# Kernel optimization log

Hardware: AMD Instinct MI355X
Metric: run time of the kernel (lower is better)

## Reference

```python
import jax, jax.numpy as jnp
import numpy as np

H = 16      # num_attention_heads
HD = 32     # attention_head_size
W = 7       # window size (per side)
N = W * W   # tokens per window = 49
MW = 64     # windows per image (mask_shape)
C = H * HD  # dim = 512
B = 2048    # total windows = images * MW


def _relative_position_index():
    coords = np.stack(np.meshgrid(np.arange(W), np.arange(W), indexing='ij'))  # [2,W,W]
    cf = coords.reshape(2, -1)                      # [2, N]
    rel = cf[:, :, None] - cf[:, None, :]           # [2, N, N]
    rel = rel.transpose(1, 2, 0).copy()             # [N, N, 2]
    rel[:, :, 0] += W - 1
    rel[:, :, 1] += W - 1
    rel[:, :, 0] *= 2 * W - 1
    return jnp.asarray(rel.sum(-1), dtype=jnp.int32)  # [N, N] indices into bias table

REL_IDX = _relative_position_index()


def setup_inputs() -> dict:
    key = jax.random.key(0)
    ks = jax.random.split(key, 9)
    s = 0.02
    return {
        "hidden_states": jax.random.normal(ks[0], (B, N, C), jnp.float32),
        "attention_mask": jax.random.normal(ks[1], (MW, N, N), jnp.float32),
        "wq": jax.random.normal(ks[2], (C, C), jnp.float32) * s,
        "bq": jax.random.normal(ks[3], (C,), jnp.float32) * s,
        "wk": jax.random.normal(ks[4], (C, C), jnp.float32) * s,
        "bk": jax.random.normal(ks[5], (C,), jnp.float32) * s,
        "wv": jax.random.normal(ks[6], (C, C), jnp.float32) * s,
        "bv": jax.random.normal(ks[7], (C,), jnp.float32) * s,
        "bias_table": jax.random.normal(ks[8], ((2 * W - 1) ** 2, H), jnp.float32) * s,
    }


def reference(hidden_states, attention_mask, wq, bq, wk, bk, wv, bv, bias_table):
    # hidden_states: [B, N, C]
    def proj(w, b):
        y = hidden_states @ w.T + b                  # [B, N, C]
        return y.reshape(B, N, H, HD).transpose(0, 2, 1, 3)  # [B, H, N, HD]

    q = proj(wq, bq)
    k = proj(wk, bk)
    v = proj(wv, bv)

    inv_sqrt_d = 1.0 / jnp.sqrt(jnp.float32(HD))
    scores = jnp.einsum('bhnd,bhmd->bhnm', q, k) * inv_sqrt_d  # [B, H, N, N]

    # relative position bias gather: [N, N, H] -> [H, N, N]
    rel_bias = bias_table[REL_IDX].transpose(2, 0, 1)
    scores = scores + rel_bias[None]

    # shifted-window mask: broadcast over image groups and heads
    scores = scores.reshape(B // MW, MW, H, N, N) + attention_mask[None, :, None]
    scores = scores.reshape(B, H, N, N)

    probs = jax.nn.softmax(scores, axis=-1)
    ctx = jnp.einsum('bhnm,bhmd->bhnd', probs, v)    # [B, H, N, HD]
    return ctx.transpose(0, 2, 1, 3).reshape(B, N, C)
```

## Files before the change

### kernel.cpp

```cpp
#include <hip/hip_runtime.h>
#include <hip/hip_bf16.h>
#include <string.h>

typedef unsigned short u16;
typedef __attribute__((ext_vector_type(8))) short short8;
typedef __attribute__((ext_vector_type(4))) float floatx4;
typedef __attribute__((ext_vector_type(4))) unsigned short ushort4v;
typedef __attribute__((ext_vector_type(8))) unsigned short ushort8v;
typedef __attribute__((ext_vector_type(2))) unsigned int uint2v;

#define NWIN 2048
#define NTOK 49
#define NH 16
#define HDIM 32
#define CDIM 512
#define MTOT (NWIN * NTOK)
#define NOUT (3 * CDIM)
#define KDIM CDIM

__device__ inline float b2f(u16 u) {
    unsigned int x = ((unsigned int)u) << 16;
    float f; __builtin_memcpy(&f, &x, 4); return f;
}
__device__ inline u16 f2b(float f) {
    unsigned int u; __builtin_memcpy(&u, &f, 4);
    unsigned int r = (u + 0x7fffu + ((u >> 16) & 1u)) >> 16;
    return (u16)r;
}
__device__ inline void gload16(const void* g, void* l) {
    __builtin_amdgcn_global_load_lds((const __attribute__((address_space(1))) unsigned int*)g,
                                     (__attribute__((address_space(3))) unsigned int*)l, 16, 0, 0);
}

__global__ void k_cvt_x(const float4* __restrict__ x, ushort4v* __restrict__ xb, int n4) {
    int i = blockIdx.x * blockDim.x + threadIdx.x;
    int stride = gridDim.x * blockDim.x;
    for (; i < n4; i += stride) {
        float4 v = x[i];
        ushort4v o = { f2b(v.x), f2b(v.y), f2b(v.z), f2b(v.w) };
        xb[i] = o;
    }
}

__global__ void k_pack_w(const float* __restrict__ wq, const float* __restrict__ wk,
                         const float* __restrict__ wv, const float* __restrict__ bq,
                         const float* __restrict__ bk, const float* __restrict__ bv,
                         u16* __restrict__ wout, float* __restrict__ bout) {
    const int WN = CDIM * CDIM;
    int i = blockIdx.x * blockDim.x + threadIdx.x;
    if (i < 3 * WN) {
        const float* src = (i < WN) ? wq : (i < 2 * WN ? wk : wv);
        wout[i] = f2b(src[i & (WN - 1)]);
    }
    if (i < 3 * CDIM) {
        const float* sb = (i < CDIM) ? bq : (i < 2 * CDIM ? bk : bv);
        bout[i] = sb[i & (CDIM - 1)];
    }
}

__global__ void k_bm(const float* __restrict__ mask, const float* __restrict__ bt,
                     float* __restrict__ bm) {
    int t = blockIdx.x;
    int w = t >> 4, h = t & 15;
    for (int e = threadIdx.x; e < NTOK * NTOK; e += blockDim.x) {
        int j = e / 49, i = e - j * 49;
        int ri = i / 7, ci = i - ri * 7;
        int rj = j / 7, cj = j - rj * 7;
        int idx = (ri - rj + 6) * 13 + (ci - cj + 6);
        bm[(size_t)t * 2401 + e] = bt[idx * 16 + h] + mask[(size_t)w * 2401 + i * 49 + j];
    }
}

__global__ __launch_bounds__(512, 2)
void k_gemm256(const u16* __restrict__ A, const u16* __restrict__ Bw,
               const float* __restrict__ bias, u16* __restrict__ C) {
    __shared__ __align__(16) u16 lds[65536];
    const int tid = threadIdx.x;
    const int lane = tid & 63;
    const int wave = tid >> 6;
    const int wm = wave >> 2;
    const int wn = wave & 3;
    const int c = lane & 15;
    const int quad = lane >> 4;

    const int wg = blockIdx.x;
    const int swz = (wg & 7) * 294 + (wg >> 3);
    const int m0 = (swz / 6) * 256;
    const int n0 = (swz % 6) * 256;

    const int r1 = tid >> 3;
    const int cg = ((tid & 7) ^ (r1 & 7)) * 8;
    const int bpr = (r1 & 15) * 4 + (r1 >> 4);
    const u16* pA00 = A + (size_t)(m0 + r1) * KDIM + cg;
    const u16* pA01 = A + (size_t)(m0 + 64 + r1) * KDIM + cg;
    const u16* pA10 = A + (size_t)(m0 + 128 + r1) * KDIM + cg;
    const u16* pA11 = A + (size_t)(m0 + 192 + r1) * KDIM + cg;
    const u16* pB00 = Bw + (size_t)(n0 + bpr) * KDIM + cg;
    const u16* pB01 = Bw + (size_t)(n0 + 64 + bpr) * KDIM + cg;
    const u16* pB10 = Bw + (size_t)(n0 + 128 + bpr) * KDIM + cg;
    const u16* pB11 = Bw + (size_t)(n0 + 192 + bpr) * KDIM + cg;

#define STG(P0, P1, BUFU, HALFU, KOFF) \
    gload16(P0 + (KOFF), lds + (BUFU) + (HALFU) + tid * 8); \
    gload16(P1 + (KOFF), lds + (BUFU) + (HALFU) + 4096 + tid * 8);
#define STG_A0(T)  STG(pA00, pA01, 0, 0, (T)*64)
#define STG_A1(T)  STG(pA10, pA11, 0, 8192, (T)*64)
#define STG_B0(T)  STG(pB00, pB01, 0, 16384, (T)*64)
#define STG_B1(T)  STG(pB10, pB11, 0, 24576, (T)*64)
#define STG_A0b(T) STG(pA00, pA01, 32768, 0, (T)*64)
#define STG_A1b(T) STG(pA10, pA11, 32768, 8192, (T)*64)
#define STG_B0b(T) STG(pB00, pB01, 32768, 16384, (T)*64)
#define STG_B1b(T) STG(pB10, pB11, 32768, 24576, (T)*64)

    const char* ldsc = (const char*)lds;
    const int aBase = wm * 16384;
    const int bBase = 32768 + (wn >> 1) * 16384 + (wn & 1) * 8192;
    const int cx = (c & 7) << 4;
    const int kq0 = (quad * 16) ^ cx;
    const int kq1 = (64 + quad * 16) ^ cx;

    short8 af[4][2];
    short8 bf[2][2][2];
    floatx4 acc[8][4];
#pragma unroll
    for (int mf = 0; mf < 8; mf++)
#pragma unroll
        for (int nf = 0; nf < 4; nf++)
            acc[mf][nf] = (floatx4){0.f, 0.f, 0.f, 0.f};

#define LDA(BUF, MH) { _Pragma("unroll") for (int mi = 0; mi < 4; mi++) { \
        const char* pp_ = ldsc + (BUF)*65536 + aBase + (MH)*8192 + (mi*16 + c)*128; \
        af[mi][0] = *(const short8*)(pp_ + kq0); \
        af[mi][1] = *(const short8*)(pp_ + kq1); } }
#define LDB(BUF, NH) { _Pragma("unroll") for (int ni = 0; ni < 2; ni++) { \
        const char* pp_ = ldsc + (BUF)*65536 + bBase + (NH)*4096 + (ni*16 + c)*128; \
        bf[NH][ni][0] = *(const short8*)(pp_ + kq0); \
        bf[NH][ni][1] = *(const short8*)(pp_ + kq1); } }
#define BAR __builtin_amdgcn_s_barrier()
#define WAITLGKM { asm volatile("s_waitcnt lgkmcnt(0)" ::: "memory"); __builtin_amdgcn_sched_barrier(0); }
#define MQ(MH, NH) do { __builtin_amdgcn_s_setprio(1); \
    _Pragma("unroll") for (int kk = 0; kk < 2; kk++) \
    _Pragma("unroll") for (int mi = 0; mi < 4; mi++) \
    _Pragma("unroll") for (int ni = 0; ni < 2; ni++) \
        acc[(MH)*4 + mi][(NH)*2 + ni] = __builtin_amdgcn_mfma_f32_16x16x32_bf16( \
            af[mi][kk], bf[NH][ni][kk], acc[(MH)*4 + mi][(NH)*2 + ni], 0, 0, 0); \
    __builtin_amdgcn_s_setprio(0); } while (0)

#define GITER(T2, T3, ST, VM4) \
     LDA(0,0); LDB(0,0);                               BAR; WAITLGKM; MQ(0,0); BAR; \
     LDB(0,1);                                         BAR; WAITLGKM; MQ(0,1); BAR; \
     LDA(0,1); if (ST) { STG_B0(T2); }                 BAR; WAITLGKM; MQ(1,0); BAR; \
     if (ST) { STG_B1(T2); STG_A0(T2); }               BAR; WAITLGKM; MQ(1,1); \
            asm volatile("s_waitcnt " VM4 ::: "memory");      BAR; \
     LDA(1,0); LDB(1,0); if (ST) { STG_A1(T2); }       BAR; WAITLGKM; MQ(0,0); BAR; \
     LDB(1,1);                                         BAR; WAITLGKM; MQ(0,1); BAR; \
     LDA(1,1); if (ST) { STG_B0b(T3); }                BAR; WAITLGKM; MQ(1,0); BAR; \
     if (ST) { STG_B1b(T3); STG_A0b(T3); STG_A1b(T3); } BAR; WAITLGKM; MQ(1,1); \
            if (ST) { asm volatile("s_waitcnt vmcnt(8)" ::: "memory"); } BAR;

    STG_A0(0); STG_A1(0); STG_B0(0); STG_B1(0);
    STG_A0b(1); STG_A1b(1); STG_B0b(1); STG_B1b(1);
    asm volatile("s_waitcnt vmcnt(8)" ::: "memory");
    BAR;

    GITER(2, 3, 1, "vmcnt(6)")
    GITER(4, 5, 1, "vmcnt(6)")
    GITER(6, 7, 1, "vmcnt(6)")
    GITER(8, 9, 0, "vmcnt(0)")

    const float4 bb = *(const float4*)&bias[n0 + wn * 64 + c * 4];
    u16* cbase = C + (size_t)(m0 + wm * 128 + quad * 4) * NOUT + n0 + wn * 64 + c * 4;
#pragma unroll
    for (int mf = 0; mf < 8; mf++) {
#pragma unroll
        for (int r = 0; r < 4; r++) {
            float x0 = acc[mf][0][r] + bb.x;
            float x1 = acc[mf][1][r] + bb.y;
            float x2 = acc[mf][2][r] + bb.z;
            float x3 = acc[mf][3][r] + bb.w;
            unsigned int d0, d1;
            asm("v_cvt_pk_bf16_f32 %0, %1, %2" : "=v"(d0) : "v"(x0), "v"(x1));
            asm("v_cvt_pk_bf16_f32 %0, %1, %2" : "=v"(d1) : "v"(x2), "v"(x3));
            uint2v w2 = { d0, d1 };
            *(uint2v*)(cbase + (size_t)(mf * 16 + r) * NOUT) = w2;
        }
    }
#undef STG
#undef STG_A0
#undef STG_A1
#undef STG_B0
#undef STG_B1
#undef STG_A0b
#undef STG_A1b
#undef STG_B0b
#undef STG_B1b
#undef LDA
#undef LDB
#undef BAR
#undef WAITLGKM
#undef MQ
#undef GITER
}

__global__ __launch_bounds__(256, 3)
void k_attn(const u16* __restrict__ qkv, const float* __restrict__ bmT,
            float* __restrict__ out) {
    __shared__ __align__(16) char smem[4 * 12288];
    const int lane = threadIdx.x & 63;
    const int wave = threadIdx.x >> 6;
    const int task = blockIdx.x * 4 + wave;
    const int b = task >> 4;
    const int h = task & 15;
    const int c = lane & 15;
    const int quad = lane >> 4;
    char* Vs = smem + wave * 12288;
    char* Ps = Vs + 4096;

    const u16* qbase = qkv + (size_t)b * NTOK * NOUT + h * 32;

    short8 kf[4], qf[4];
#pragma unroll
    for (int mi = 0; mi < 4; mi++) {
        int jr = mi * 16 + c; jr = jr > 48 ? 48 : jr;
        kf[mi] = *(const short8*)(qbase + (size_t)jr * NOUT + 512 + quad * 8);
    }
#pragma unroll
    for (int ni = 0; ni < 4; ni++) {
        int ir = ni * 16 + c; ir = ir > 48 ? 48 : ir;
        qf[ni] = *(const short8*)(qbase + (size_t)ir * NOUT + quad * 8);
    }

#pragma unroll
    for (int it = 0; it < 4; it++) {
        int j = it * 16 + (lane >> 2);
        int part = lane & 3;
        ushort8v val = {0, 0, 0, 0, 0, 0, 0, 0};
        if (j < 49) val = *(const ushort8v*)(qbase + (size_t)j * NOUT + 1024 + part * 8);
        int byt = (j * 64 + part * 16) ^ (((j >> 3) & 3) << 4);
        *(ushort8v*)(Vs + byt) = val;
    }

    floatx4 acc[4][4];
#pragma unroll
    for (int mi = 0; mi < 4; mi++)
#pragma unroll
        for (int ni = 0; ni < 4; ni++)
            acc[mi][ni] = (floatx4){0.f, 0.f, 0.f, 0.f};
#pragma unroll
    for (int mi = 0; mi < 4; mi++)
#pragma unroll
        for (int ni = 0; ni < 4; ni++)
            acc[mi][ni] = __builtin_amdgcn_mfma_f32_16x16x32_bf16(kf[mi], qf[ni], acc[mi][ni], 0, 0, 0);

    const float scale = 0.17677669529663687f;
    const float* bmrow = bmT + ((size_t)((b & 63) * 16 + h)) * 2401;
#pragma unroll
    for (int mi = 0; mi < 4; mi++)
#pragma unroll
        for (int r = 0; r < 4; r++) {
            int j = mi * 16 + quad * 4 + r;
            int jc = j > 48 ? 48 : j;
            const float* bp = bmrow + jc * 49;
#pragma unroll
            for (int ni = 0; ni < 4; ni++) {
                int i = ni * 16 + c;
                int ic = i > 48 ? 48 : i;
                acc[mi][ni][r] = acc[mi][ni][r] * scale + bp[ic];
            }
        }

#pragma unroll
    for (int ni = 0; ni < 4; ni++) {
        float mx = -3.0e38f;
#pragma unroll
        for (int mi = 0; mi < 3; mi++)
#pragma unroll
            for (int r = 0; r < 4; r++) mx = fmaxf(mx, acc[mi][ni][r]);
        if (quad == 0) mx = fmaxf(mx, acc[3][ni][0]);
        mx = fmaxf(mx, __shfl_xor(mx, 16));
        mx = fmaxf(mx, __shfl_xor(mx, 32));
        float sum = 0.f;
#pragma unroll
        for (int mi = 0; mi < 3; mi++)
#pragma unroll
            for (int r = 0; r < 4; r++) {
                float e = __expf(acc[mi][ni][r] - mx);
                acc[mi][ni][r] = e; sum += e;
            }
        float e0 = (quad == 0) ? __expf(acc[3][ni][0] - mx) : 0.f;
        acc[3][ni][0] = e0; sum += e0;
        acc[3][ni][1] = 0.f; acc[3][ni][2] = 0.f; acc[3][ni][3] = 0.f;
        sum += __shfl_xor(sum, 16);
        sum += __shfl_xor(sum, 32);
        float inv = 1.0f / sum;
#pragma unroll
        for (int mi = 0; mi < 4; mi++)
#pragma unroll
            for (int r = 0; r < 4; r++) acc[mi][ni][r] *= inv;
    }

    const int cx = (c & 7) << 4;
#pragma unroll
    for (int ni = 0; ni < 4; ni++) {
        char* prow = Ps + (ni * 16 + c) * 128;
#pragma unroll
        for (int mi = 0; mi < 4; mi++) {
            unsigned int d0, d1;
            asm("v_cvt_pk_bf16_f32 %0, %1, %2" : "=v"(d0) : "v"(acc[mi][ni][0]), "v"(acc[mi][ni][1]));
            asm("v_cvt_pk_bf16_f32 %0, %1, %2" : "=v"(d1) : "v"(acc[mi][ni][2]), "v"(acc[mi][ni][3]));
            uint2v w2 = { d0, d1 };
            *(uint2v*)(prow + ((mi * 32 + quad * 8) ^ cx)) = w2;
        }
    }

    asm volatile("s_waitcnt lgkmcnt(0)" ::: "memory");

    floatx4 acc2[4][2];
#pragma unroll
    for (int mi = 0; mi < 4; mi++)
#pragma unroll
        for (int ni = 0; ni < 2; ni++) acc2[mi][ni] = (floatx4){0.f, 0.f, 0.f, 0.f};
    const int vb0 = quad * 512 + (((0 * 16 + c) * 2) ^ (quad << 4));
    const int vb1 = quad * 512 + (((1 * 16 + c) * 2) ^ (quad << 4));
#pragma unroll
    for (int kk = 0; kk < 2; kk++) {
        const int plow = (kk * 64 + quad * 16) ^ cx;
        short8 pf[4];
#pragma unroll
        for (int mi = 0; mi < 4; mi++)
            pf[mi] = *(const short8*)(Ps + mi * 2048 + c * 128 + plow);
        short8 vf[2];
#pragma unroll
        for (int ni = 0; ni < 2; ni++) {
            const char* vbp = Vs + (ni ? vb1 : vb0) + kk * 2048;
#pragma unroll
            for (int z = 0; z < 8; z++)
                vf[ni][z] = *(const short*)(vbp + z * 64);
        }
#pragma unroll
        for (int mi = 0; mi < 4; mi++)
#pragma unroll
            for (int ni = 0; ni < 2; ni++)
                acc2[mi][ni] = __builtin_amdgcn_mfma_f32_16x16x32_bf16(pf[mi], vf[ni], acc2[mi][ni], 0, 0, 0);
    }

    float* ob = out + (size_t)b * 49 * CDIM + h * 32;
#pragma unroll
    for (int mi = 0; mi < 4; mi++)
#pragma unroll
        for (int r = 0; r < 4; r++) {
            int i = mi * 16 + quad * 4 + r;
            if (i < 49) {
                float* orow = ob + (size_t)i * CDIM + c;
#pragma unroll
                for (int ni = 0; ni < 2; ni++)
                    orow[ni * 16] = acc2[mi][ni][r];
            }
        }
}

extern "C" void kernel_launch(void* const* d_in, const int* in_sizes, int n_in,
                              void* d_out, int out_size, void* d_ws, size_t ws_size,
                              hipStream_t stream) {
    const float* hs   = (const float*)d_in[0];
    const float* mask = (const float*)d_in[1];
    const float* wq   = (const float*)d_in[2];
    const float* bq   = (const float*)d_in[3];
    const float* wk   = (const float*)d_in[4];
    const float* bk   = (const float*)d_in[5];
    const float* wv   = (const float*)d_in[6];
    const float* bv   = (const float*)d_in[7];
    const float* bt   = (const float*)d_in[8];
    float* out = (float*)d_out;

    char* ws = (char*)d_ws;
    size_t off = 0;
    u16* xb = (u16*)(ws + off);      off += (size_t)MTOT * CDIM * 2;
    u16* wb = (u16*)(ws + off);      off += (size_t)NOUT * KDIM * 2;
    float* biasb = (float*)(ws + off); off += (size_t)NOUT * 4;
    off = (off + 255) & ~(size_t)255;
    float* bm = (float*)(ws + off);  off += (size_t)1024 * 2401 * 4;
    off = (off + 255) & ~(size_t)255;
    u16* qkv = (u16*)(ws + off);     off += (size_t)MTOT * NOUT * 2;

    k_cvt_x<<<4096, 256, 0, stream>>>((const float4*)hs, (ushort4v*)xb, MTOT * CDIM / 4);
    k_pack_w<<<3072, 256, 0, stream>>>(wq, wk, wv, bq, bk, bv, wb, biasb);
    k_bm<<<1024, 256, 0, stream>>>(mask, bt, bm);
    k_gemm256<<<2352, 512, 0, stream>>>(xb, wb, biasb, qkv);
    k_attn<<<8192, 256, 0, stream>>>(qkv, bm, out);
}
```

Measured before the change: 648.1 us.

## Fuse fp32-to-bf16 activation conversion into QKV GEMM A-tile loading

Removes the separate k_cvt_x kernel and its bf16 workspace buffer. The GEMM now loads fp32 hidden states into registers, packs them to bf16 with v_cvt_pk_bf16_f32 and writes them to LDS, while B still uses direct global-to-LDS loads. This saves one full write and read of the converted activation matrix. In exchange the A traffic inside the GEMM doubles, A staging costs extra registers and VALU work, and the pipeline's vmcnt waits had to be rebalanced.

```diff
diff --git a/kernel.cpp b/kernel.cpp
--- a/kernel.cpp
+++ b/kernel.cpp
@@ -8,6 +8,7 @@
 typedef __attribute__((ext_vector_type(4))) unsigned short ushort4v;
 typedef __attribute__((ext_vector_type(8))) unsigned short ushort8v;
 typedef __attribute__((ext_vector_type(2))) unsigned int uint2v;
+typedef __attribute__((ext_vector_type(4))) unsigned int uint4v;
 
 #define NWIN 2048
 #define NTOK 49
@@ -31,15 +32,14 @@
     __builtin_amdgcn_global_load_lds((const __attribute__((address_space(1))) unsigned int*)g,
                                      (__attribute__((address_space(3))) unsigned int*)l, 16, 0, 0);
 }
-
-__global__ void k_cvt_x(const float4* __restrict__ x, ushort4v* __restrict__ xb, int n4) {
-    int i = blockIdx.x * blockDim.x + threadIdx.x;
-    int stride = gridDim.x * blockDim.x;
-    for (; i < n4; i += stride) {
-        float4 v = x[i];
-        ushort4v o = { f2b(v.x), f2b(v.y), f2b(v.z), f2b(v.w) };
-        xb[i] = o;
-    }
+__device__ inline uint4v pkrow(float4 x, float4 y) {
+    unsigned int o0, o1, o2, o3;
+    asm("v_cvt_pk_bf16_f32 %0, %1, %2" : "=v"(o0) : "v"(x.x), "v"(x.y));
+    asm("v_cvt_pk_bf16_f32 %0, %1, %2" : "=v"(o1) : "v"(x.z), "v"(x.w));
+    asm("v_cvt_pk_bf16_f32 %0, %1, %2" : "=v"(o2) : "v"(y.x), "v"(y.y));
+    asm("v_cvt_pk_bf16_f32 %0, %1, %2" : "=v"(o3) : "v"(y.z), "v"(y.w));
+    uint4v o = { o0, o1, o2, o3 };
+    return o;
 }
 
 __global__ void k_pack_w(const float* __restrict__ wq, const float* __restrict__ wk,
@@ -72,7 +72,7 @@
 }
 
 __global__ __launch_bounds__(512, 2)
-void k_gemm256(const u16* __restrict__ A, const u16* __restrict__ Bw,
+void k_gemm256(const float* __restrict__ Aw, const u16* __restrict__ Bw,
                const float* __restrict__ bias, u16* __restrict__ C) {
     __shared__ __align__(16) u16 lds[65536];
     const int tid = threadIdx.x;
@@ -91,26 +91,35 @@
     const int r1 = tid >> 3;
     const int cg = ((tid & 7) ^ (r1 & 7)) * 8;
     const int bpr = (r1 & 15) * 4 + (r1 >> 4);
-    const u16* pA00 = A + (size_t)(m0 + r1) * KDIM + cg;
-    const u16* pA01 = A + (size_t)(m0 + 64 + r1) * KDIM + cg;
-    const u16* pA10 = A + (size_t)(m0 + 128 + r1) * KDIM + cg;
-    const u16* pA11 = A + (size_t)(m0 + 192 + r1) * KDIM + cg;
+    const float* pAlo = Aw + (size_t)(m0 + r1) * KDIM + cg;
+    const float* pAhi = Aw + (size_t)(m0 + 128 + r1) * KDIM + cg;
     const u16* pB00 = Bw + (size_t)(n0 + bpr) * KDIM + cg;
     const u16* pB01 = Bw + (size_t)(n0 + 64 + bpr) * KDIM + cg;
     const u16* pB10 = Bw + (size_t)(n0 + 128 + bpr) * KDIM + cg;
     const u16* pB11 = Bw + (size_t)(n0 + 192 + bpr) * KDIM + cg;
 
-#define STG(P0, P1, BUFU, HALFU, KOFF) \
+#define STGB(P0, P1, BUFU, HALFU, KOFF) \
     gload16(P0 + (KOFF), lds + (BUFU) + (HALFU) + tid * 8); \
     gload16(P1 + (KOFF), lds + (BUFU) + (HALFU) + 4096 + tid * 8);
-#define STG_A0(T)  STG(pA00, pA01, 0, 0, (T)*64)
-#define STG_A1(T)  STG(pA10, pA11, 0, 8192, (T)*64)
-#define STG_B0(T)  STG(pB00, pB01, 0, 16384, (T)*64)
-#define STG_B1(T)  STG(pB10, pB11, 0, 24576, (T)*64)
-#define STG_A0b(T) STG(pA00, pA01, 32768, 0, (T)*64)
-#define STG_A1b(T) STG(pA10, pA11, 32768, 8192, (T)*64)
-#define STG_B0b(T) STG(pB00, pB01, 32768, 16384, (T)*64)
-#define STG_B1b(T) STG(pB10, pB11, 32768, 24576, (T)*64)
+#define STG_B0(T)  STGB(pB00, pB01, 0, 16384, (T)*64)
+#define STG_B1(T)  STGB(pB10, pB11, 0, 24576, (T)*64)
+#define STG_B0b(T) STGB(pB00, pB01, 32768, 16384, (T)*64)
+#define STG_B1b(T) STGB(pB10, pB11, 32768, 24576, (T)*64)
+
+    float4 gA0, gA1, gA2, gA3;
+    float4 gB0, gB1, gB2, gB3;
+#define GLA_LO(T) { const float* p_ = pAlo + (T)*64; \
+    gA0 = *(const float4*)p_;       gA1 = *(const float4*)(p_ + 4); \
+    gA2 = *(const float4*)(p_ + 64*KDIM); gA3 = *(const float4*)(p_ + 64*KDIM + 4); }
+#define GLA_HI(T) { const float* p_ = pAhi + (T)*64; \
+    gB0 = *(const float4*)p_;       gB1 = *(const float4*)(p_ + 4); \
+    gB2 = *(const float4*)(p_ + 64*KDIM); gB3 = *(const float4*)(p_ + 64*KDIM + 4); }
+#define WRA_LO(BUFU) { \
+    *(uint4v*)(lds + (BUFU) + tid * 8)        = pkrow(gA0, gA1); \
+    *(uint4v*)(lds + (BUFU) + 4096 + tid * 8) = pkrow(gA2, gA3); }
+#define WRA_HI(BUFU) { \
+    *(uint4v*)(lds + (BUFU) + 8192 + tid * 8)  = pkrow(gB0, gB1); \
+    *(uint4v*)(lds + (BUFU) + 12288 + tid * 8) = pkrow(gB2, gB3); }
 
     const char* ldsc = (const char*)lds;
     const int aBase = wm * 16384;
@@ -145,28 +154,35 @@
         acc[(MH)*4 + mi][(NH)*2 + ni] = __builtin_amdgcn_mfma_f32_16x16x32_bf16( \
             af[mi][kk], bf[NH][ni][kk], acc[(MH)*4 + mi][(NH)*2 + ni], 0, 0, 0); \
     __builtin_amdgcn_s_setprio(0); } while (0)
+#define VMC(N) asm volatile("s_waitcnt vmcnt(" #N ")" ::: "memory")
 
 #define GITER(T2, T3, ST, VM4) \
-     LDA(0,0); LDB(0,0);                               BAR; WAITLGKM; MQ(0,0); BAR; \
-     LDB(0,1);                                         BAR; WAITLGKM; MQ(0,1); BAR; \
-     LDA(0,1); if (ST) { STG_B0(T2); }                 BAR; WAITLGKM; MQ(1,0); BAR; \
-     if (ST) { STG_B1(T2); STG_A0(T2); }               BAR; WAITLGKM; MQ(1,1); \
-            asm volatile("s_waitcnt " VM4 ::: "memory");      BAR; \
-     LDA(1,0); LDB(1,0); if (ST) { STG_A1(T2); }       BAR; WAITLGKM; MQ(0,0); BAR; \
-     LDB(1,1);                                         BAR; WAITLGKM; MQ(0,1); BAR; \
-     LDA(1,1); if (ST) { STG_B0b(T3); }                BAR; WAITLGKM; MQ(1,0); BAR; \
-     if (ST) { STG_B1b(T3); STG_A0b(T3); STG_A1b(T3); } BAR; WAITLGKM; MQ(1,1); \
-            if (ST) { asm volatile("s_waitcnt vmcnt(8)" ::: "memory"); } BAR;
-
-    STG_A0(0); STG_A1(0); STG_B0(0); STG_B1(0);
-    STG_A0b(1); STG_A1b(1); STG_B0b(1); STG_B1b(1);
-    asm volatile("s_waitcnt vmcnt(8)" ::: "memory");
+     LDA(0,0); LDB(0,0); if (ST) { GLA_LO(T2); }   BAR; WAITLGKM; MQ(0,0); BAR; \
+     LDB(0,1); if (ST) { GLA_HI(T2); }             BAR; WAITLGKM; MQ(0,1); BAR; \
+     LDA(0,1); if (ST) { STG_B0(T2); }             BAR; WAITLGKM; MQ(1,0); BAR; \
+     if (ST) { STG_B1(T2); }                       BAR; WAITLGKM; MQ(1,1); \
+            VM4; if (ST) { WRA_LO(0); }                   BAR; \
+     LDA(1,0); LDB(1,0); if (ST) { GLA_LO(T3); }   BAR; WAITLGKM; MQ(0,0); \
+            if (ST) { VMC(8); WRA_HI(0); }                BAR; \
+     LDB(1,1); if (ST) { GLA_HI(T3); }             BAR; WAITLGKM; MQ(0,1); BAR; \
+     LDA(1,1); if (ST) { STG_B0b(T3); }            BAR; WAITLGKM; MQ(1,0); BAR; \
+     if (ST) { STG_B1b(T3); }                      BAR; WAITLGKM; MQ(1,1); \
+            if (ST) { VMC(4); WRA_LO(32768); WRA_HI(32768); } BAR;
+
+    GLA_LO(0); GLA_HI(0);
+    STG_B0(0); STG_B1(0); STG_B0b(1); STG_B1b(1);
+    VMC(8);
+    WRA_LO(0); WRA_HI(0);
+    GLA_LO(1); GLA_HI(1);
+    VMC(0);
+    WRA_LO(32768); WRA_HI(32768);
+    asm volatile("s_waitcnt lgkmcnt(0)" ::: "memory");
     BAR;
 
-    GITER(2, 3, 1, "vmcnt(6)")
-    GITER(4, 5, 1, "vmcnt(6)")
-    GITER(6, 7, 1, "vmcnt(6)")
-    GITER(8, 9, 0, "vmcnt(0)")
+    GITER(2, 3, 1, VMC(8))
+    GITER(4, 5, 1, VMC(8))
+    GITER(6, 7, 1, VMC(8))
+    GITER(8, 9, 0, VMC(0))
 
     const float4 bb = *(const float4*)&bias[n0 + wn * 64 + c * 4];
     u16* cbase = C + (size_t)(m0 + wm * 128 + quad * 4) * NOUT + n0 + wn * 64 + c * 4;
@@ -185,20 +201,21 @@
             *(uint2v*)(cbase + (size_t)(mf * 16 + r) * NOUT) = w2;
         }
     }
-#undef STG
-#undef STG_A0
-#undef STG_A1
+#undef STGB
 #undef STG_B0
 #undef STG_B1
-#undef STG_A0b
-#undef STG_A1b
 #undef STG_B0b
 #undef STG_B1b
+#undef GLA_LO
+#undef GLA_HI
+#undef WRA_LO
+#undef WRA_HI
 #undef LDA
 #undef LDB
 #undef BAR
 #undef WAITLGKM
 #undef MQ
+#undef VMC
 #undef GITER
 }
 
@@ -375,7 +392,6 @@
 
     char* ws = (char*)d_ws;
     size_t off = 0;
-    u16* xb = (u16*)(ws + off);      off += (size_t)MTOT * CDIM * 2;
     u16* wb = (u16*)(ws + off);      off += (size_t)NOUT * KDIM * 2;
     float* biasb = (float*)(ws + off); off += (size_t)NOUT * 4;
     off = (off + 255) & ~(size_t)255;
@@ -383,9 +399,8 @@
     off = (off + 255) & ~(size_t)255;
     u16* qkv = (u16*)(ws + off);     off += (size_t)MTOT * NOUT * 2;
 
-    k_cvt_x<<<4096, 256, 0, stream>>>((const float4*)hs, (ushort4v*)xb, MTOT * CDIM / 4);
     k_pack_w<<<3072, 256, 0, stream>>>(wq, wk, wv, bq, bk, bv, wb, biasb);
     k_bm<<<1024, 256, 0, stream>>>(mask, bt, bm);
-    k_gemm256<<<2352, 512, 0, stream>>>(xb, wb, biasb, qkv);
+    k_gemm256<<<2352, 512, 0, stream>>>(hs, wb, biasb, qkv);
     k_attn<<<8192, 256, 0, stream>>>(qkv, bm, out);
 }
```

New measurement: 660.5 us. About the same (+1.9%).
